# Kernel tuning notes

Hardware: AMD Instinct MI355X
Metric: run time of the kernel (lower is better)

Reference implementation:

```python
import jax, jax.numpy as jnp
import numpy as np

W0, W1 = 14, 14            # window size
NUM_HEADS = 12
DIM = 768
HEAD_DIM = DIM // NUM_HEADS
N_TOK = W0 * W1 + 1        # 197 (with cls token)
BATCH = 64


def _mask_1d_rel_pos_index(s):
    i = np.arange(s)
    return i[None, :] - i[:, None] + s - 1


def _add_cls(index, num_tokens, offset):
    index = index.reshape(num_tokens, num_tokens)
    new = np.zeros((num_tokens + 1, num_tokens + 1), dtype=np.int32)
    new[1:, 1:] = index
    new[0, :] = offset
    new[:, 0] = offset + 1
    new[0, 0] = offset + 2
    return new


def _build_rel_indices():
    nt = W0 * W1
    h = _mask_1d_rel_pos_index(W0).reshape(W0, 1, W0, 1)
    h = np.broadcast_to(h, (W0, W1, W0, W1))
    h_index = _add_cls(h, nt, 2 * W0 - 1)
    w = _mask_1d_rel_pos_index(W1).reshape(1, W1, 1, W1)
    w = np.broadcast_to(w, (W0, W1, W0, W1))
    w_index = _add_cls(w, nt, 2 * W1 - 1)
    return jnp.asarray(h_index), jnp.asarray(w_index)


def setup_inputs() -> dict:
    key = jax.random.key(0)
    ks = jax.random.split(key, 6)
    h_index, w_index = _build_rel_indices()
    return {
        "x": jax.random.normal(ks[0], (BATCH, N_TOK, DIM), dtype=jnp.float32),
        "qkv_w": jax.random.normal(ks[1], (3 * DIM, DIM), dtype=jnp.float32) * 0.02,
        "q_bias": jnp.zeros((DIM,), dtype=jnp.float32),
        "v_bias": jnp.zeros((DIM,), dtype=jnp.float32),
        "proj_w": jax.random.normal(ks[2], (DIM, DIM), dtype=jnp.float32) * 0.02,
        "proj_b": jnp.zeros((DIM,), dtype=jnp.float32),
        "rpb_high": jax.random.normal(ks[3], (2 * W0 + 2, NUM_HEADS), dtype=jnp.float32) * 0.02,
        "rpb_width": jax.random.normal(ks[4], (2 * W1 + 2, NUM_HEADS), dtype=jnp.float32) * 0.02,
        "h_index": h_index,
        "w_index": w_index,
    }


def reference(x, qkv_w, q_bias, v_bias, proj_w, proj_b, rpb_high, rpb_width,
              h_index, w_index):
    B, N, C = x.shape
    scale = HEAD_DIM ** (-0.5)
    # fused qkv with (q_bias, 0, v_bias) bias as in torch source
    bias = jnp.concatenate([q_bias, jnp.zeros_like(v_bias), v_bias])
    qkv = x @ qkv_w.T + bias                             # [B, N, 3*C]
    qkv = qkv.reshape(B, N, 3, NUM_HEADS, HEAD_DIM).transpose(2, 0, 3, 1, 4)
    q, k, v = qkv[0], qkv[1], qkv[2]                     # [B, H, N, hd]
    q = q * scale
    # qk_float=True -> scores in float32
    attn = jnp.einsum('bhnd,bhmd->bhnm',
                      q.astype(jnp.float32), k.astype(jnp.float32))
    # decoupled relative position bias: two embedding lookups, summed
    rpb = rpb_high[h_index] + rpb_width[w_index]         # [N, N, H]
    rpb = rpb.transpose(2, 0, 1)                         # [H, N, N]
    attn = attn + rpb[None].astype(attn.dtype)
    attn = jax.nn.softmax(attn, axis=-1).astype(x.dtype)
    out = jnp.einsum('bhnm,bhmd->bnhd', attn, v).reshape(B, N, C)
    return out @ proj_w.T + proj_b
```

## Files before the change

### kernel.cpp

```cpp
#include <hip/hip_runtime.h>
#include <hip/hip_bf16.h>
#include <cstdint>
#include <cstddef>

using fx4  = __attribute__((ext_vector_type(4))) float;
using bfx8 = __attribute__((ext_vector_type(8))) short;
using sx4  = __attribute__((ext_vector_type(4))) short;

#define DEV __device__ __forceinline__

static constexpr int BATCH = 64;
static constexpr int NTOK  = 197;
static constexpr int NH    = 12;
static constexpr int HD    = 64;
static constexpr int MROWS = BATCH * NTOK;
static constexpr int MPAD  = 12800;
static constexpr int KDIM  = 768;

DEV unsigned short f2bf(float f) {
  unsigned u = __builtin_bit_cast(unsigned, f);
  u += 0x7FFFu + ((u >> 16) & 1u);
  return (unsigned short)(u >> 16);
}

DEV void gload16(const unsigned short* g, unsigned short* l) {
  __builtin_amdgcn_global_load_lds(
      (const __attribute__((address_space(1))) unsigned int*)g,
      (__attribute__((address_space(3))) unsigned int*)l, 16, 0, 0);
}

DEV int xcd_swizzle(int orig, int nwg) {
  int q = nwg >> 3, r = nwg & 7;
  int xcd = orig & 7, lid = orig >> 3;
  return (xcd < r ? xcd * (q + 1) : r * (q + 1) + (xcd - r) * q) + lid;
}

__global__ void rpb_kernel(const float* __restrict__ rh, const float* __restrict__ rw,
                           const int* __restrict__ hidx, const int* __restrict__ widx,
                           float* __restrict__ rpb)
{
  int e = blockIdx.x * 256 + threadIdx.x;
  const int NN = NTOK * NTOK;
  if (e >= NH * NN) return;
  int h = e / NN, ij = e % NN;
  rpb[e] = rh[hidx[ij] * NH + h] + rw[widx[ij] * NH + h];
}

__global__ void cvt_kernel(const float* __restrict__ in,
                           unsigned short* __restrict__ out,
                           int nvec, int nvec_pad)
{
  for (int v = blockIdx.x * 256 + threadIdx.x; v < nvec_pad; v += gridDim.x * 256) {
    fx4 x = (v < nvec) ? ((const fx4*)in)[v] : fx4{0.f, 0.f, 0.f, 0.f};
    sx4 h4;
    #pragma unroll
    for (int q = 0; q < 4; q++) h4[q] = (short)f2bf(x[q]);
    ((sx4*)out)[v] = h4;
  }
}

template<int NT, int MODE>
__global__ __launch_bounds__(256, 4)
void gemm_bf16_kernel(const unsigned short* __restrict__ A,
                      const unsigned short* __restrict__ B,
                      const float* __restrict__ bias0, const float* __restrict__ bias1,
                      unsigned short* __restrict__ qb, unsigned short* __restrict__ kb,
                      unsigned short* __restrict__ vb, float* __restrict__ outp)
{
  __shared__ unsigned short At[128 * 32];
  __shared__ unsigned short Bt[128 * 32];

  const int t  = threadIdx.x;
  const int w  = t >> 6, l = t & 63;
  const int wr = w >> 1, wc = w & 1;
  const int fr = l & 15, g = l >> 4;
  const int bid = xcd_swizzle(blockIdx.x, gridDim.x);
  const int bm = bid / NT, bn = bid % NT;

  const int r_issue = l >> 2;
  const int c_us    = (l & 3) * 8;

  fx4 acc[4][4];
  #pragma unroll
  for (int i = 0; i < 4; i++)
    #pragma unroll
    for (int j = 0; j < 4; j++) acc[i][j] = fx4{0.f, 0.f, 0.f, 0.f};

  #pragma unroll 1
  for (int kt = 0; kt < 24; kt++) {
    const int k0 = kt * 32;

    __syncthreads();
    #pragma unroll
    for (int e2 = 0; e2 < 2; e2++) {
      int e = w * 2 + e2;
      int arow = bm * 128 + e * 16 + r_issue;
      gload16(A + (size_t)arow * KDIM + k0 + c_us, &At[e * 512]);
      int brow = bn * 128 + e * 16 + r_issue;
      gload16(B + (size_t)brow * KDIM + k0 + c_us, &Bt[e * 512]);
    }
    __syncthreads();

    bfx8 fa[4], fb[4];
    #pragma unroll
    for (int i = 0; i < 4; i++)
      fa[i] = *(const bfx8*)&At[(wr * 64 + i * 16 + fr) * 32 + g * 8];
    #pragma unroll
    for (int j = 0; j < 4; j++)
      fb[j] = *(const bfx8*)&Bt[(wc * 64 + j * 16 + fr) * 32 + g * 8];
    #pragma unroll
    for (int i = 0; i < 4; i++)
      #pragma unroll
      for (int j = 0; j < 4; j++)
        acc[i][j] = __builtin_amdgcn_mfma_f32_16x16x32_bf16(fa[i], fb[j], acc[i][j], 0, 0, 0);
  }

  #pragma unroll
  for (int i = 0; i < 4; i++) {
    #pragma unroll
    for (int j = 0; j < 4; j++) {
      #pragma unroll
      for (int r = 0; r < 4; r++) {
        int row = bm * 128 + wr * 64 + i * 16 + g * 4 + r;
        int col = bn * 128 + wc * 64 + j * 16 + fr;
        if (row >= MROWS) continue;
        float v = acc[i][j][r];
        if (MODE == 0) {
          int which = col / 768;
          int hh = (col >> 6) % 12;
          int d  = col & 63;
          int b  = row / NTOK, n = row % NTOK;
          size_t o = (((size_t)(b * NH + hh)) * NTOK + n) * HD + d;
          if (which == 0)      qb[o] = f2bf((v + bias0[col]) * 0.125f);
          else if (which == 1) kb[o] = f2bf(v);
          else                 vb[o] = f2bf(v + bias1[col - 1536]);
        } else {
          outp[(size_t)row * 768 + col] = v + bias0[col];
        }
      }
    }
  }
}

__global__ __launch_bounds__(256)
void attn_mfma_kernel(const unsigned short* __restrict__ qf,
                      const unsigned short* __restrict__ kf,
                      const unsigned short* __restrict__ vf,
                      const float* __restrict__ rpb,
                      unsigned short* __restrict__ of)
{
  __shared__ union {
    short Kb[224 * 72];
    struct { short Pb[64 * 232]; short Vt[32 * 232]; } p;
  } u;

  const int t  = threadIdx.x;
  const int w  = t >> 6, l = t & 63;
  const int fr = l & 15, g = l >> 4;
  const int bx = xcd_swizzle(blockIdx.x, BATCH * NH * 4);
  const int b  = bx / (NH * 4);
  const int h  = (bx / 4) % NH;
  const int qt = bx & 3;
  const size_t base = ((size_t)(b * NH + h)) * NTOK * HD;
  const unsigned short* qg = qf + base;
  const unsigned short* kg = kf + base;
  const unsigned short* vg = vf + base;
  const float* rhb = rpb + (size_t)h * (NTOK * NTOK);

  const bfx8 z8 = bfx8{0,0,0,0,0,0,0,0};
  const int qrow0 = qt * 64 + w * 16 + g * 4;

  fx4 sc[14];
  #pragma unroll
  for (int j = 0; j < 14; j++) {
    int key = j * 16 + fr;
    #pragma unroll
    for (int r = 0; r < 4; r++) {
      int qrow = qrow0 + r;
      sc[j][r] = (key < NTOK && qrow < NTOK) ? rhb[qrow * NTOK + key] : 0.f;
    }
  }

  const int qrow_f = qt * 64 + w * 16 + fr;
  bfx8 aq0 = z8, aq1 = z8;
  if (qrow_f < NTOK) {
    aq0 = *(const bfx8*)(qg + (size_t)qrow_f * HD + g * 8);
    aq1 = *(const bfx8*)(qg + (size_t)qrow_f * HD + 32 + g * 8);
  }

  sx4 vreg[7];
  const int vm  = (7 * 256 + 0, t);
  auto VLOAD = [&](int hf) {
    #pragma unroll
    for (int rep = 0; rep < 7; rep++) {
      int task = rep * 256 + t;
      int m  = task >> 3;
      int dq = task & 7;
      vreg[rep] = (m < NTOK)
          ? *(const sx4*)(vg + (size_t)m * HD + hf * 32 + dq * 4)
          : sx4{0, 0, 0, 0};
    }
  };
  auto VWRITE = [&]() {
    #pragma unroll
    for (int rep = 0; rep < 7; rep++) {
      int task = rep * 256 + t;
      int m  = task >> 3;
      int dq = task & 7;
      #pragma unroll
      for (int q2 = 0; q2 < 4; q2++)
        u.p.Vt[(dq * 4 + q2) * 232 + m] = vreg[rep][q2];
    }
  };

  VLOAD(0);

  {
    const int rr = t >> 3, c8 = (t & 7) * 8;
    #pragma unroll
    for (int p = 0; p < 7; p++) {
      int r = p * 32 + rr;
      bfx8 o8 = (r < NTOK) ? *(const bfx8*)(kg + (size_t)r * HD + c8) : z8;
      *(bfx8*)&u.Kb[r * 72 + c8] = o8;
    }
  }
  __syncthreads();

  #pragma unroll
  for (int j = 0; j < 14; j++) {
    bfx8 k0 = *(const bfx8*)&u.Kb[(j * 16 + fr) * 72 + g * 8];
    bfx8 k1 = *(const bfx8*)&u.Kb[(j * 16 + fr) * 72 + 32 + g * 8];
    sc[j] = __builtin_amdgcn_mfma_f32_16x16x32_bf16(aq0, k0, sc[j], 0, 0, 0);
    sc[j] = __builtin_amdgcn_mfma_f32_16x16x32_bf16(aq1, k1, sc[j], 0, 0, 0);
  }

  #pragma unroll
  for (int j = 12; j < 14; j++) {
    int key = j * 16 + fr;
    if (key >= NTOK) {
      #pragma unroll
      for (int r = 0; r < 4; r++) sc[j][r] = -1e30f;
    }
  }

  float inv4[4];
  #pragma unroll
  for (int r = 0; r < 4; r++) {
    float m = sc[0][r];
    #pragma unroll
    for (int j = 1; j < 14; j++) m = fmaxf(m, sc[j][r]);
    #pragma unroll
    for (int off = 1; off < 16; off <<= 1) m = fmaxf(m, __shfl_xor(m, off));
    float sum = 0.f;
    #pragma unroll
    for (int j = 0; j < 14; j++) {
      float e = __expf(sc[j][r] - m);
      sc[j][r] = e; sum += e;
    }
    #pragma unroll
    for (int off = 1; off < 16; off <<= 1) sum += __shfl_xor(sum, off);
    inv4[r] = 1.0f / sum;
  }

  __syncthreads();

  #pragma unroll
  for (int j = 0; j < 14; j++) {
    int key = j * 16 + fr;
    #pragma unroll
    for (int r = 0; r < 4; r++)
      u.p.Pb[(w * 16 + g * 4 + r) * 232 + key] = (short)f2bf(sc[j][r]);
  }
  VWRITE();
  __syncthreads();

  fx4 o2[4];
  #pragma unroll
  for (int j = 0; j < 4; j++) o2[j] = fx4{0.f, 0.f, 0.f, 0.f};

  VLOAD(1);

  #pragma unroll
  for (int kc = 0; kc < 7; kc++) {
    bfx8 pa = *(const bfx8*)&u.p.Pb[(w * 16 + fr) * 232 + kc * 32 + g * 8];
    #pragma unroll
    for (int jj = 0; jj < 2; jj++) {
      bfx8 vbb = *(const bfx8*)&u.p.Vt[(jj * 16 + fr) * 232 + kc * 32 + g * 8];
      o2[jj] = __builtin_amdgcn_mfma_f32_16x16x32_bf16(pa, vbb, o2[jj], 0, 0, 0);
    }
  }

  __syncthreads();
  VWRITE();
  __syncthreads();

  #pragma unroll
  for (int kc = 0; kc < 7; kc++) {
    bfx8 pa = *(const bfx8*)&u.p.Pb[(w * 16 + fr) * 232 + kc * 32 + g * 8];
    #pragma unroll
    for (int jj = 0; jj < 2; jj++) {
      bfx8 vbb = *(const bfx8*)&u.p.Vt[(jj * 16 + fr) * 232 + kc * 32 + g * 8];
      o2[2 + jj] = __builtin_amdgcn_mfma_f32_16x16x32_bf16(pa, vbb, o2[2 + jj], 0, 0, 0);
    }
  }

  #pragma unroll
  for (int r = 0; r < 4; r++) {
    int qrow = qt * 64 + w * 16 + g * 4 + r;
    if (qrow < NTOK) {
      float inv = inv4[r];
      #pragma unroll
      for (int j = 0; j < 4; j++)
        of[((size_t)(b * NTOK + qrow)) * 768 + h * 64 + j * 16 + fr]
            = f2bf(o2[j][r] * inv);
    }
  }
  (void)vm;
}

extern "C" void kernel_launch(void* const* d_in, const int* in_sizes, int n_in,
                              void* d_out, int out_size, void* d_ws, size_t ws_size,
                              hipStream_t stream)
{
  const float* x      = (const float*)d_in[0];
  const float* qkv_w  = (const float*)d_in[1];
  const float* q_bias = (const float*)d_in[2];
  const float* v_bias = (const float*)d_in[3];
  const float* proj_w = (const float*)d_in[4];
  const float* proj_b = (const float*)d_in[5];
  const float* rpb_h  = (const float*)d_in[6];
  const float* rpb_w  = (const float*)d_in[7];
  const int*   h_idx  = (const int*)d_in[8];
  const int*   w_idx  = (const int*)d_in[9];
  float* out = (float*)d_out;

  char* ws = (char*)d_ws;
  size_t off = 0;
  auto alloc = [&](size_t bytes) { size_t o = off; off += (bytes + 255) & ~(size_t)255; return o; };

  const size_t QKV_ELEMS = (size_t)BATCH * NH * NTOK * HD;
  unsigned short* Axb = (unsigned short*)(ws + alloc((size_t)MPAD * KDIM * 2));
  unsigned short* Bqb = (unsigned short*)(ws + alloc((size_t)2304 * KDIM * 2));
  unsigned short* Bpb = (unsigned short*)(ws + alloc((size_t)768 * KDIM * 2));
  unsigned short* qb  = (unsigned short*)(ws + alloc(QKV_ELEMS * 2));
  unsigned short* kb  = (unsigned short*)(ws + alloc(QKV_ELEMS * 2));
  unsigned short* vb  = (unsigned short*)(ws + alloc(QKV_ELEMS * 2));
  float*          rpb = (float*)(ws + alloc((size_t)NH * NTOK * NTOK * 4));
  unsigned short* ofb = (unsigned short*)(ws + alloc((size_t)MPAD * KDIM * 2));
  (void)ws_size; (void)in_sizes; (void)n_in; (void)out_size;

  const int nvec_x  = MROWS * KDIM / 4;
  const int nvec_xp = MPAD * KDIM / 4;

  cvt_kernel<<<2048, 256, 0, stream>>>(x, Axb, nvec_x, nvec_xp);
  cvt_kernel<<<1024, 256, 0, stream>>>(qkv_w, Bqb, 2304 * KDIM / 4, 2304 * KDIM / 4);
  cvt_kernel<<<512, 256, 0, stream>>>(proj_w, Bpb, 768 * KDIM / 4, 768 * KDIM / 4);
  {
    int total = NH * NTOK * NTOK;
    rpb_kernel<<<(total + 255) / 256, 256, 0, stream>>>(rpb_h, rpb_w, h_idx, w_idx, rpb);
  }
  hipMemsetAsync(ofb + (size_t)MROWS * KDIM, 0,
                 (size_t)(MPAD - MROWS) * KDIM * 2, stream);
  gemm_bf16_kernel<18, 0><<<99 * 18, 256, 0, stream>>>(
      Axb, Bqb, q_bias, v_bias, qb, kb, vb, nullptr);
  attn_mfma_kernel<<<BATCH * NH * 4, 256, 0, stream>>>(qb, kb, vb, rpb, ofb);
  gemm_bf16_kernel<6, 1><<<99 * 6, 256, 0, stream>>>(
      ofb, Bpb, proj_b, nullptr, nullptr, nullptr, nullptr, out);
}
```

Before: 193.1 us.

## Enlarge GEMM tiles to 256x128x64 with 512 threads and XOR-swizzled LDS

Both bf16 GEMMs now use 512-thread blocks that compute a 256x128 output tile, so each block covers twice as many rows and B tiles are reused more. The K-step grows from 32 to 64, halving the number of barrier-separated stage iterations. LDS rows are stored with an XOR chunk swizzle to avoid bank conflicts on the fragment reads. The trade-offs are larger LDS use (48KB per block) and register pressure, which may lower occupancy, and a coarser grid that can load-balance worse, especially for the small projection GEMM.

```diff
diff --git a/kernel.cpp b/kernel.cpp
--- a/kernel.cpp
+++ b/kernel.cpp
@@ -60,15 +60,15 @@
 }
 
 template<int NT, int MODE>
-__global__ __launch_bounds__(256, 4)
+__global__ __launch_bounds__(512, 4)
 void gemm_bf16_kernel(const unsigned short* __restrict__ A,
                       const unsigned short* __restrict__ B,
                       const float* __restrict__ bias0, const float* __restrict__ bias1,
                       unsigned short* __restrict__ qb, unsigned short* __restrict__ kb,
                       unsigned short* __restrict__ vb, float* __restrict__ outp)
 {
-  __shared__ unsigned short At[128 * 32];
-  __shared__ unsigned short Bt[128 * 32];
+  __shared__ unsigned short At[256 * 64];
+  __shared__ unsigned short Bt[128 * 64];
 
   const int t  = threadIdx.x;
   const int w  = t >> 6, l = t & 63;
@@ -77,8 +77,21 @@
   const int bid = xcd_swizzle(blockIdx.x, gridDim.x);
   const int bm = bid / NT, bn = bid % NT;
 
-  const int r_issue = l >> 2;
-  const int c_us    = (l & 3) * 8;
+  const int srow = w * 8 + (l >> 3);
+  const int sgr8 = ((l & 7) ^ ((l >> 3) & 7)) * 8;
+
+  auto STAGE = [&](int k0) {
+    #pragma unroll
+    for (int rd = 0; rd < 4; rd++) {
+      int arow = bm * 256 + rd * 64 + srow;
+      gload16(A + (size_t)arow * KDIM + k0 + sgr8, &At[(rd * 512 + w * 64) * 8]);
+    }
+    #pragma unroll
+    for (int rd = 0; rd < 2; rd++) {
+      int brow = bn * 128 + rd * 64 + srow;
+      gload16(B + (size_t)brow * KDIM + k0 + sgr8, &Bt[(rd * 512 + w * 64) * 8]);
+    }
+  };
 
   fx4 acc[4][4];
   #pragma unroll
@@ -86,33 +99,31 @@
     #pragma unroll
     for (int j = 0; j < 4; j++) acc[i][j] = fx4{0.f, 0.f, 0.f, 0.f};
 
+  const int a_r0 = wr * 64 + fr;
+  const int b_r0 = wc * 64 + fr;
+  const int swz7 = fr & 7;
+
   #pragma unroll 1
-  for (int kt = 0; kt < 24; kt++) {
-    const int k0 = kt * 32;
-
+  for (int kt = 0; kt < 12; kt++) {
     __syncthreads();
-    #pragma unroll
-    for (int e2 = 0; e2 < 2; e2++) {
-      int e = w * 2 + e2;
-      int arow = bm * 128 + e * 16 + r_issue;
-      gload16(A + (size_t)arow * KDIM + k0 + c_us, &At[e * 512]);
-      int brow = bn * 128 + e * 16 + r_issue;
-      gload16(B + (size_t)brow * KDIM + k0 + c_us, &Bt[e * 512]);
-    }
+    STAGE(kt * 64);
     __syncthreads();
 
-    bfx8 fa[4], fb[4];
-    #pragma unroll
-    for (int i = 0; i < 4; i++)
-      fa[i] = *(const bfx8*)&At[(wr * 64 + i * 16 + fr) * 32 + g * 8];
-    #pragma unroll
-    for (int j = 0; j < 4; j++)
-      fb[j] = *(const bfx8*)&Bt[(wc * 64 + j * 16 + fr) * 32 + g * 8];
-    #pragma unroll
-    for (int i = 0; i < 4; i++)
+    #pragma unroll
+    for (int ks = 0; ks < 2; ks++) {
+      const int gsw = ((ks * 4 + g) ^ swz7) * 8;
+      bfx8 fb[4];
       #pragma unroll
       for (int j = 0; j < 4; j++)
-        acc[i][j] = __builtin_amdgcn_mfma_f32_16x16x32_bf16(fa[i], fb[j], acc[i][j], 0, 0, 0);
+        fb[j] = *(const bfx8*)&Bt[(b_r0 + j * 16) * 64 + gsw];
+      #pragma unroll
+      for (int i = 0; i < 4; i++) {
+        bfx8 fa = *(const bfx8*)&At[(a_r0 + i * 16) * 64 + gsw];
+        #pragma unroll
+        for (int j = 0; j < 4; j++)
+          acc[i][j] = __builtin_amdgcn_mfma_f32_16x16x32_bf16(fa, fb[j], acc[i][j], 0, 0, 0);
+      }
+    }
   }
 
   #pragma unroll
@@ -121,7 +132,7 @@
     for (int j = 0; j < 4; j++) {
       #pragma unroll
       for (int r = 0; r < 4; r++) {
-        int row = bm * 128 + wr * 64 + i * 16 + g * 4 + r;
+        int row = bm * 256 + wr * 64 + i * 16 + g * 4 + r;
         int col = bn * 128 + wc * 64 + j * 16 + fr;
         if (row >= MROWS) continue;
         float v = acc[i][j][r];
@@ -189,7 +200,6 @@
   }
 
   sx4 vreg[7];
-  const int vm  = (7 * 256 + 0, t);
   auto VLOAD = [&](int hf) {
     #pragma unroll
     for (int rep = 0; rep < 7; rep++) {
@@ -315,7 +325,6 @@
             = f2bf(o2[j][r] * inv);
     }
   }
-  (void)vm;
 }
 
 extern "C" void kernel_launch(void* const* d_in, const int* in_sizes, int n_in,
@@ -361,9 +370,9 @@
   }
   hipMemsetAsync(ofb + (size_t)MROWS * KDIM, 0,
                  (size_t)(MPAD - MROWS) * KDIM * 2, stream);
-  gemm_bf16_kernel<18, 0><<<99 * 18, 256, 0, stream>>>(
+  gemm_bf16_kernel<18, 0><<<50 * 18, 512, 0, stream>>>(
       Axb, Bqb, q_bias, v_bias, qb, kb, vb, nullptr);
   attn_mfma_kernel<<<BATCH * NH * 4, 256, 0, stream>>>(qb, kb, vb, rpb, ofb);
-  gemm_bf16_kernel<6, 1><<<99 * 6, 256, 0, stream>>>(
+  gemm_bf16_kernel<6, 1><<<50 * 6, 512, 0, stream>>>(
       ofb, Bpb, proj_b, nullptr, nullptr, nullptr, nullptr, out);
 }
```

New measurement: 177.1 us. -8.3%, faster.
